# Kernel tuning notes

Hardware: AMD Instinct MI355X
Metric: run time of the kernel (lower is better)

Reference implementation:

```python
import jax, jax.numpy as jnp
import numpy as np
from jax import lax

HEADS = 4
DIM_HEAD = 32
IH = IW = 64
IH_RED = 32  # image_size // reduce_ratio; F.interpolate(size=int) -> square output


def dw_conv(t, w):
    # depthwise 3x3, stride 1, padding 1, NCHW; w: [C,1,3,3]
    return lax.conv_general_dilated(t, w, (1, 1), [(1, 1), (1, 1)],
                                    feature_group_count=t.shape[1],
                                    dimension_numbers=("NCHW", "OIHW", "NCHW"))


def pw_conv(t, w):
    # pointwise 1x1 conv as einsum; w: [O,C,1,1]
    return jnp.einsum("oc,bchw->bohw", w[:, :, 0, 0], t)


def resize_bilinear_ac(t, out_h, out_w):
    # bilinear, align_corners=True, t: [B,C,H,W]
    H, W = t.shape[-2], t.shape[-1]
    ys = jnp.linspace(0.0, H - 1.0, out_h)
    xs = jnp.linspace(0.0, W - 1.0, out_w)
    y0 = jnp.floor(ys).astype(jnp.int32)
    x0 = jnp.floor(xs).astype(jnp.int32)
    y1 = jnp.minimum(y0 + 1, H - 1)
    x1 = jnp.minimum(x0 + 1, W - 1)
    wy = (ys - y0).astype(t.dtype)[None, None, :, None]
    wx = (xs - x0).astype(t.dtype)[None, None, None, :]
    row = t[:, :, y0, :] * (1 - wy) + t[:, :, y1, :] * wy  # [B,C,OH,W]
    out = row[:, :, :, x0] * (1 - wx) + row[:, :, :, x1] * wx  # [B,C,OH,OW]
    return out


def to_heads(t):
    # [B, h*d, H, W] -> [B, h, H*W, d]
    B, _, H, W = t.shape
    return t.reshape(B, HEADS, DIM_HEAD, H * W).transpose(0, 1, 3, 2)


def setup_inputs() -> dict:
    key = jax.random.key(0)
    ks = jax.random.split(key, 7)
    inner = HEADS * DIM_HEAD  # 128
    return {
        "x": jax.random.normal(ks[0], (8, 256, 16, 16), jnp.float32),
        "skip": jax.random.normal(ks[1], (8, 128, 64, 64), jnp.float32),
        "dw_q": jax.random.normal(ks[2], (128, 1, 3, 3), jnp.float32) * 0.1,
        "pw_q": jax.random.normal(ks[3], (inner, 128, 1, 1), jnp.float32) * 0.05,
        "dw_kv": jax.random.normal(ks[4], (256, 1, 3, 3), jnp.float32) * 0.1,
        "pw_kv": jax.random.normal(ks[5], (2 * inner, 256, 1, 1), jnp.float32) * 0.05,
        "w_out": jax.random.normal(ks[6], (128, inner, 1, 1), jnp.float32) * 0.05,
    }


def reference(x, skip, dw_q, pw_q, dw_kv, pw_kv, w_out):
    scale = DIM_HEAD ** -0.5
    q = to_heads(pw_conv(dw_conv(skip, dw_q), pw_q))  # [B,h,4096,d]
    kv = pw_conv(dw_conv(x, dw_kv), pw_kv)            # [B,2*inner,16,16]
    k, v = jnp.split(kv, 2, axis=1)
    k = to_heads(resize_bilinear_ac(k, IH_RED, IH_RED))  # [B,h,1024,d]
    v = to_heads(resize_bilinear_ac(v, IH_RED, IH_RED))
    dots = jnp.einsum("bhqd,bhkd->bhqk", q, k) * scale
    attn = jax.nn.softmax(dots, axis=-1)
    out = jnp.einsum("bhqk,bhkd->bhqd", attn, v)  # [B,h,4096,d]
    B = out.shape[0]
    out = out.transpose(0, 1, 3, 2).reshape(B, HEADS * DIM_HEAD, IH, IW)
    return pw_conv(out, w_out)
```

## Files before the change

### kernel.cpp

```cpp
#include <hip/hip_runtime.h>
#include <hip/hip_bf16.h>

typedef __attribute__((ext_vector_type(4))) float f32x4;
typedef __attribute__((ext_vector_type(8))) short bf16x8;
typedef __attribute__((ext_vector_type(4))) unsigned u32x4;

#define DEV static __device__ __forceinline__

DEV int imin(int a, int b) { return a < b ? a : b; }

DEV short f2bf(float f) {
  union { float f; unsigned u; } v; v.f = f;
  unsigned r = (v.u + 0x7fffu + ((v.u >> 16) & 1u)) >> 16;
  return (short)r;
}

DEV unsigned pkbf(float lo, float hi) {
  unsigned r;
  asm("v_cvt_pk_bf16_f32 %0, %1, %2" : "=v"(r) : "v"(lo), "v"(hi));
  return r;
}

DEV bf16x8 cvt8(const float* __restrict__ p) {
  f32x4 a = *reinterpret_cast<const f32x4*>(p);
  f32x4 b = *reinterpret_cast<const f32x4*>(p + 4);
  bf16x8 r;
  r[0] = f2bf(a[0]); r[1] = f2bf(a[1]); r[2] = f2bf(a[2]); r[3] = f2bf(a[3]);
  r[4] = f2bf(b[0]); r[5] = f2bf(b[1]); r[6] = f2bf(b[2]); r[7] = f2bf(b[3]);
  return r;
}

DEV int sigma(int s) { return ((s & 4) << 2) | ((s >> 3) << 2) | (s & 3); }

__global__ __launch_bounds__(256) void k_dwq(const float* __restrict__ skip,
    const float* __restrict__ dw_q, short* __restrict__ dwQ) {
  const int b = blockIdx.z, cq = blockIdx.y, y = blockIdx.x;
  __shared__ __align__(16) short T[64][40];
  const int t = threadIdx.x;
  {
    const int x = t & 63, cg = t >> 6;
    #pragma unroll
    for (int i = 0; i < 8; ++i) {
      const int cl = cg * 8 + i;
      const int c = cq * 32 + cl;
      const float* sp = skip + (b * 128 + c) * 4096;
      const float* wp = dw_q + c * 9;
      float acc = 0.f;
      #pragma unroll
      for (int ky = 0; ky < 3; ++ky) {
        const int yy = y + ky - 1;
        if (yy < 0 || yy > 63) continue;
        #pragma unroll
        for (int kx = 0; kx < 3; ++kx) {
          const int xx = x + kx - 1;
          if (xx < 0 || xx > 63) continue;
          acc += sp[yy * 64 + xx] * wp[ky * 3 + kx];
        }
      }
      T[x][cl] = f2bf(acc);
    }
  }
  __syncthreads();
  const int x2 = t >> 2, cc = t & 3;
  bf16x8 v = *reinterpret_cast<const bf16x8*>(&T[x2][cc * 8]);
  *reinterpret_cast<bf16x8*>(dwQ + (b * 4096 + y * 64 + x2) * 128 + cq * 32 + cc * 8) = v;
}

__global__ __launch_bounds__(512) void k_kvgen(const float* __restrict__ x,
    const float* __restrict__ dw_kv, const float* __restrict__ pw_kv,
    float* __restrict__ kv16) {
  const int b = blockIdx.y;
  const int pq = blockIdx.x;
  __shared__ __align__(16) short dwxT[16][264];
  const int t = threadIdx.x;
  {
    const int pl = t & 15;
    const int cg = t >> 4;
    const int py = pq, px = pl;
    #pragma unroll
    for (int i = 0; i < 8; ++i) {
      const int c = cg * 8 + i;
      const float* sp = x + (b * 256 + c) * 256;
      const float* wp = dw_kv + c * 9;
      float acc = 0.f;
      #pragma unroll
      for (int ky = 0; ky < 3; ++ky) {
        const int yy = py + ky - 1;
        if (yy < 0 || yy > 15) continue;
        #pragma unroll
        for (int kx = 0; kx < 3; ++kx) {
          const int xx = px + kx - 1;
          if (xx < 0 || xx > 15) continue;
          acc += sp[yy * 16 + xx] * wp[ky * 3 + kx];
        }
      }
      dwxT[pl][c] = f2bf(acc);
    }
  }
  __syncthreads();
  const int w = t >> 6, l = t & 63, lr = l & 15, lg = l >> 4;
  f32x4 acc[2];
  #pragma unroll
  for (int ot = 0; ot < 2; ++ot) acc[ot] = f32x4{0.f, 0.f, 0.f, 0.f};
  #pragma unroll
  for (int kk = 0; kk < 8; ++kk) {
    const int c0 = kk * 32 + lg * 8;
    bf16x8 bfr = *reinterpret_cast<const bf16x8*>(&dwxT[lr][c0]);
    #pragma unroll
    for (int ot = 0; ot < 2; ++ot) {
      const int o = (w * 2 + ot) * 16 + lr;
      bf16x8 afr = cvt8(pw_kv + o * 256 + c0);
      acc[ot] = __builtin_amdgcn_mfma_f32_16x16x32_bf16(afr, bfr, acc[ot], 0, 0, 0);
    }
  }
  #pragma unroll
  for (int ot = 0; ot < 2; ++ot)
    #pragma unroll
    for (int r = 0; r < 4; ++r) {
      const int o = (w * 2 + ot) * 16 + lg * 4 + r;
      const int pix = pq * 16 + lr;
      kv16[(b * 256 + o) * 256 + pix] = acc[ot][r];
    }
}

DEV float bilin16(const float* __restrict__ p, int key) {
  const int oy = key >> 5, ox = key & 31;
  const float s = 15.f / 31.f;
  const float syf = oy * s, sxf = ox * s;
  const int y0 = (int)syf, x0 = (int)sxf;
  const int y1 = imin(y0 + 1, 15), x1 = imin(x0 + 1, 15);
  const float wy = syf - (float)y0, wx = sxf - (float)x0;
  const float r0 = p[y0 * 16 + x0] * (1.f - wx) + p[y0 * 16 + x1] * wx;
  const float r1 = p[y1 * 16 + x0] * (1.f - wx) + p[y1 * 16 + x1] * wx;
  return r0 * (1.f - wy) + r1 * wy;
}

__global__ __launch_bounds__(256) void k_resize(const float* __restrict__ kv16,
    short* __restrict__ Kp, short* __restrict__ Vp) {
  const int idx = blockIdx.x * 256 + threadIdx.x;
  {
    const int pos = idx & 31;
    int rest = idx >> 5;
    const int key = rest & 1023; rest >>= 10;
    const int h = rest & 3; const int b = rest >> 2;
    const int ch = h * 32 + sigma(pos);
    Kp[idx] = f2bf(bilin16(kv16 + (b * 256 + ch) * 256, key));
  }
  {
    const int keypos = idx & 1023;
    int rest = idx >> 10;
    const int d = rest & 31; rest >>= 5;
    const int h = rest & 3; const int b = rest >> 2;
    const int key = (keypos & ~31) | sigma(keypos & 31);
    const int ch = 128 + h * 32 + d;
    Vp[idx] = f2bf(bilin16(kv16 + (b * 256 + ch) * 256, key));
  }
}

__global__ __launch_bounds__(256) void k_attn(const short* __restrict__ dwQ,
    const float* __restrict__ pw_q, const short* __restrict__ Kp,
    const short* __restrict__ Vp, const float* __restrict__ w_out,
    float* __restrict__ out) {
  const int b = blockIdx.y;
  const int q0 = blockIdx.x * 32;
  const int t = threadIdx.x, h = t >> 6, l = t & 63;
  const int lr = l & 15, lg = l >> 4;
  __shared__ __align__(16) short QT[32][136];
  __shared__ __align__(16) short AT[32][136];

  {
    const int rr = t >> 4, c16 = t & 15;
    #pragma unroll
    for (int i = 0; i < 2; ++i) {
      const int q = rr + i * 16;
      bf16x8 v = *reinterpret_cast<const bf16x8*>(dwQ + (b * 4096 + q0 + q) * 128 + c16 * 8);
      *reinterpret_cast<bf16x8*>(&QT[q][c16 * 8]) = v;
    }
  }
  __syncthreads();

  bf16x8 qf[2];
  {
    f32x4 aq[2][2];
    #pragma unroll
    for (int ot = 0; ot < 2; ++ot)
      #pragma unroll
      for (int qt = 0; qt < 2; ++qt) aq[ot][qt] = f32x4{0.f, 0.f, 0.f, 0.f};
    #pragma unroll
    for (int kk = 0; kk < 4; ++kk) {
      const int c0 = kk * 32 + lg * 8;
      bf16x8 bfr[2];
      #pragma unroll
      for (int qt = 0; qt < 2; ++qt)
        bfr[qt] = *reinterpret_cast<const bf16x8*>(&QT[qt * 16 + lr][c0]);
      #pragma unroll
      for (int ot = 0; ot < 2; ++ot) {
        bf16x8 afr = cvt8(pw_q + ((h * 2 + ot) * 16 + lr) * 128 + c0);
        #pragma unroll
        for (int qt = 0; qt < 2; ++qt)
          aq[ot][qt] = __builtin_amdgcn_mfma_f32_16x16x32_bf16(afr, bfr[qt], aq[ot][qt], 0, 0, 0);
      }
    }
    const float qs = 0.25505403f;
    #pragma unroll
    for (int qt = 0; qt < 2; ++qt) {
      u32x4 qw;
      qw[0] = pkbf(aq[0][qt][0] * qs, aq[0][qt][1] * qs);
      qw[1] = pkbf(aq[0][qt][2] * qs, aq[0][qt][3] * qs);
      qw[2] = pkbf(aq[1][qt][0] * qs, aq[1][qt][1] * qs);
      qw[3] = pkbf(aq[1][qt][2] * qs, aq[1][qt][3] * qs);
      qf[qt] = *reinterpret_cast<bf16x8*>(&qw);
    }
  }

  const short* Kb = Kp + (b * 4 + h) * 32768;
  const short* Vb = Vp + (b * 4 + h) * 32768;
  f32x4 oacc[2][2];
  float ls[2];
  #pragma unroll
  for (int qt = 0; qt < 2; ++qt) {
    oacc[qt][0] = f32x4{0.f, 0.f, 0.f, 0.f};
    oacc[qt][1] = f32x4{0.f, 0.f, 0.f, 0.f};
    ls[qt] = 0.f;
  }
  for (int kc = 0; kc < 1024; kc += 32) {
    bf16x8 kf[2], vf[2];
    #pragma unroll
    for (int tt = 0; tt < 2; ++tt) {
      kf[tt] = *reinterpret_cast<const bf16x8*>(Kb + (kc + tt * 16 + lr) * 32 + lg * 8);
      vf[tt] = *reinterpret_cast<const bf16x8*>(Vb + (tt * 16 + lr) * 1024 + kc + lg * 8);
    }
    #pragma unroll
    for (int qt = 0; qt < 2; ++qt) {
      const f32x4 z = f32x4{0.f, 0.f, 0.f, 0.f};
      f32x4 s0 = __builtin_amdgcn_mfma_f32_16x16x32_bf16(kf[0], qf[qt], z, 0, 0, 0);
      f32x4 s1 = __builtin_amdgcn_mfma_f32_16x16x32_bf16(kf[1], qf[qt], z, 0, 0, 0);
      float p0[4], p1[4];
      #pragma unroll
      for (int r = 0; r < 4; ++r) {
        p0[r] = __builtin_amdgcn_exp2f(s0[r]);
        p1[r] = __builtin_amdgcn_exp2f(s1[r]);
      }
      ls[qt] += ((p0[0] + p0[1]) + (p0[2] + p0[3])) + ((p1[0] + p1[1]) + (p1[2] + p1[3]));
      u32x4 pw;
      pw[0] = pkbf(p0[0], p0[1]);
      pw[1] = pkbf(p0[2], p0[3]);
      pw[2] = pkbf(p1[0], p1[1]);
      pw[3] = pkbf(p1[2], p1[3]);
      bf16x8 pf = *reinterpret_cast<bf16x8*>(&pw);
      oacc[qt][0] = __builtin_amdgcn_mfma_f32_16x16x32_bf16(pf, vf[0], oacc[qt][0], 0, 0, 0);
      oacc[qt][1] = __builtin_amdgcn_mfma_f32_16x16x32_bf16(pf, vf[1], oacc[qt][1], 0, 0, 0);
    }
  }

  #pragma unroll
  for (int qt = 0; qt < 2; ++qt) {
    float s = ls[qt];
    s += __shfl_xor(s, 16);
    s += __shfl_xor(s, 32);
    const float inv = 1.f / s;
    #pragma unroll
    for (int r = 0; r < 4; ++r) {
      const float invr = __shfl(inv, lg * 4 + r);
      const int q = qt * 16 + lg * 4 + r;
      #pragma unroll
      for (int tt = 0; tt < 2; ++tt)
        AT[q][h * 32 + tt * 16 + lr] = f2bf(oacc[qt][tt][r] * invr);
    }
  }
  __syncthreads();

  f32x4 ao[2][2];
  #pragma unroll
  for (int jt = 0; jt < 2; ++jt)
    #pragma unroll
    for (int qt = 0; qt < 2; ++qt) ao[jt][qt] = f32x4{0.f, 0.f, 0.f, 0.f};
  #pragma unroll
  for (int kk = 0; kk < 4; ++kk) {
    const int c0 = kk * 32 + lg * 8;
    bf16x8 bfr[2];
    #pragma unroll
    for (int qt = 0; qt < 2; ++qt)
      bfr[qt] = *reinterpret_cast<const bf16x8*>(&AT[qt * 16 + lr][c0]);
    #pragma unroll
    for (int jt = 0; jt < 2; ++jt) {
      bf16x8 afr = cvt8(w_out + ((h * 2 + jt) * 16 + lr) * 128 + c0);
      #pragma unroll
      for (int qt = 0; qt < 2; ++qt)
        ao[jt][qt] = __builtin_amdgcn_mfma_f32_16x16x32_bf16(afr, bfr[qt], ao[jt][qt], 0, 0, 0);
    }
  }
  #pragma unroll
  for (int jt = 0; jt < 2; ++jt)
    #pragma unroll
    for (int qt = 0; qt < 2; ++qt)
      #pragma unroll
      for (int r = 0; r < 4; ++r) {
        const int j = (h * 2 + jt) * 16 + lg * 4 + r;
        out[(b * 128 + j) * 4096 + q0 + qt * 16 + lr] = ao[jt][qt][r];
      }
}

extern "C" void kernel_launch(void* const* d_in, const int* in_sizes, int n_in,
                              void* d_out, int out_size, void* d_ws, size_t ws_size,
                              hipStream_t stream) {
  const float* x     = (const float*)d_in[0];
  const float* skip  = (const float*)d_in[1];
  const float* dw_q  = (const float*)d_in[2];
  const float* pw_q  = (const float*)d_in[3];
  const float* dw_kv = (const float*)d_in[4];
  const float* pw_kv = (const float*)d_in[5];
  const float* w_out = (const float*)d_in[6];
  float* out = (float*)d_out;
  (void)in_sizes; (void)n_in; (void)out_size; (void)ws_size;

  char* wsb = (char*)d_ws;
  short* dwQ  = (short*)(wsb);
  float* kv16 = (float*)(wsb + (size_t)(8u << 20));
  short* Kp   = (short*)(wsb + (size_t)(10u << 20));
  short* Vp   = (short*)(wsb + (size_t)(12u << 20));

  k_dwq<<<dim3(64, 4, 8), dim3(256), 0, stream>>>(skip, dw_q, dwQ);
  k_kvgen<<<dim3(16, 8), dim3(512), 0, stream>>>(x, dw_kv, pw_kv, kv16);
  k_resize<<<dim3(4096), dim3(256), 0, stream>>>(kv16, Kp, Vp);
  k_attn<<<dim3(128, 8), dim3(256), 0, stream>>>(dwQ, pw_q, Kp, Vp, w_out, out);
}
```

Measured before the change: 194.2 us.

## Split attention keys across two wave groups and halve kvgen output per block

The attention kernel now launches 512 threads per block. Each head gets two waves, and each wave handles half of the 1024 keys. The partial outputs and row sums are combined through a shared-memory pool that is reused for Q, the partials and the output tile. The output projection is also spread over all eight waves. Separately, kvgen splits its output channels across an extra grid dimension, which raises block count but makes each block recompute the depthwise conv. The intent is more waves in flight and shorter per-wave serial loops, at the cost of extra barriers and shared-memory traffic for the reduction.

```diff
diff --git a/kernel.cpp b/kernel.cpp
--- a/kernel.cpp
+++ b/kernel.cpp
@@ -69,7 +69,8 @@
 __global__ __launch_bounds__(512) void k_kvgen(const float* __restrict__ x,
     const float* __restrict__ dw_kv, const float* __restrict__ pw_kv,
     float* __restrict__ kv16) {
-  const int b = blockIdx.y;
+  const int b = blockIdx.z;
+  const int oh = blockIdx.y;
   const int pq = blockIdx.x;
   __shared__ __align__(16) short dwxT[16][264];
   const int t = threadIdx.x;
@@ -99,28 +100,20 @@
   }
   __syncthreads();
   const int w = t >> 6, l = t & 63, lr = l & 15, lg = l >> 4;
-  f32x4 acc[2];
-  #pragma unroll
-  for (int ot = 0; ot < 2; ++ot) acc[ot] = f32x4{0.f, 0.f, 0.f, 0.f};
+  f32x4 acc = f32x4{0.f, 0.f, 0.f, 0.f};
+  const int o = oh * 128 + w * 16 + lr;
   #pragma unroll
   for (int kk = 0; kk < 8; ++kk) {
     const int c0 = kk * 32 + lg * 8;
     bf16x8 bfr = *reinterpret_cast<const bf16x8*>(&dwxT[lr][c0]);
-    #pragma unroll
-    for (int ot = 0; ot < 2; ++ot) {
-      const int o = (w * 2 + ot) * 16 + lr;
-      bf16x8 afr = cvt8(pw_kv + o * 256 + c0);
-      acc[ot] = __builtin_amdgcn_mfma_f32_16x16x32_bf16(afr, bfr, acc[ot], 0, 0, 0);
-    }
-  }
-  #pragma unroll
-  for (int ot = 0; ot < 2; ++ot)
-    #pragma unroll
-    for (int r = 0; r < 4; ++r) {
-      const int o = (w * 2 + ot) * 16 + lg * 4 + r;
-      const int pix = pq * 16 + lr;
-      kv16[(b * 256 + o) * 256 + pix] = acc[ot][r];
-    }
+    bf16x8 afr = cvt8(pw_kv + o * 256 + c0);
+    acc = __builtin_amdgcn_mfma_f32_16x16x32_bf16(afr, bfr, acc, 0, 0, 0);
+  }
+  #pragma unroll
+  for (int r = 0; r < 4; ++r) {
+    const int oo = oh * 128 + w * 16 + lg * 4 + r;
+    kv16[(b * 256 + oo) * 256 + pq * 16 + lr] = acc[r];
+  }
 }
 
 DEV float bilin16(const float* __restrict__ p, int key) {
@@ -157,25 +150,25 @@
   }
 }
 
-__global__ __launch_bounds__(256) void k_attn(const short* __restrict__ dwQ,
+__global__ __launch_bounds__(512, 8) void k_attn(const short* __restrict__ dwQ,
     const float* __restrict__ pw_q, const short* __restrict__ Kp,
     const short* __restrict__ Vp, const float* __restrict__ w_out,
     float* __restrict__ out) {
   const int b = blockIdx.y;
   const int q0 = blockIdx.x * 32;
-  const int t = threadIdx.x, h = t >> 6, l = t & 63;
+  const int t = threadIdx.x, w8 = t >> 6, l = t & 63;
+  const int h = w8 & 3, ks = w8 >> 2;
   const int lr = l & 15, lg = l >> 4;
-  __shared__ __align__(16) short QT[32][136];
-  __shared__ __align__(16) short AT[32][136];
-
-  {
-    const int rr = t >> 4, c16 = t & 15;
-    #pragma unroll
-    for (int i = 0; i < 2; ++i) {
-      const int q = rr + i * 16;
-      bf16x8 v = *reinterpret_cast<const bf16x8*>(dwQ + (b * 4096 + q0 + q) * 128 + c16 * 8);
-      *reinterpret_cast<bf16x8*>(&QT[q][c16 * 8]) = v;
-    }
+  __shared__ __align__(16) char POOL[33792];
+  short* QT = (short*)POOL;
+  float* Op = (float*)POOL;
+  float* Ls = (float*)(POOL + 32768);
+  short* AT = (short*)POOL;
+
+  {
+    const int q = t >> 4, c16 = t & 15;
+    bf16x8 v = *reinterpret_cast<const bf16x8*>(dwQ + (b * 4096 + q0 + q) * 128 + c16 * 8);
+    *reinterpret_cast<bf16x8*>(&QT[q * 136 + c16 * 8]) = v;
   }
   __syncthreads();
 
@@ -192,7 +185,7 @@
       bf16x8 bfr[2];
       #pragma unroll
       for (int qt = 0; qt < 2; ++qt)
-        bfr[qt] = *reinterpret_cast<const bf16x8*>(&QT[qt * 16 + lr][c0]);
+        bfr[qt] = *reinterpret_cast<const bf16x8*>(&QT[(qt * 16 + lr) * 136 + c0]);
       #pragma unroll
       for (int ot = 0; ot < 2; ++ot) {
         bf16x8 afr = cvt8(pw_q + ((h * 2 + ot) * 16 + lr) * 128 + c0);
@@ -212,6 +205,7 @@
       qf[qt] = *reinterpret_cast<bf16x8*>(&qw);
     }
   }
+  __syncthreads();
 
   const short* Kb = Kp + (b * 4 + h) * 32768;
   const short* Vb = Vp + (b * 4 + h) * 32768;
@@ -223,7 +217,8 @@
     oacc[qt][1] = f32x4{0.f, 0.f, 0.f, 0.f};
     ls[qt] = 0.f;
   }
-  for (int kc = 0; kc < 1024; kc += 32) {
+  const int kend = ks * 512 + 512;
+  for (int kc = ks * 512; kc < kend; kc += 32) {
     bf16x8 kf[2], vf[2];
     #pragma unroll
     for (int tt = 0; tt < 2; ++tt) {
@@ -258,47 +253,55 @@
     float s = ls[qt];
     s += __shfl_xor(s, 16);
     s += __shfl_xor(s, 32);
-    const float inv = 1.f / s;
-    #pragma unroll
-    for (int r = 0; r < 4; ++r) {
-      const float invr = __shfl(inv, lg * 4 + r);
-      const int q = qt * 16 + lg * 4 + r;
-      #pragma unroll
-      for (int tt = 0; tt < 2; ++tt)
-        AT[q][h * 32 + tt * 16 + lr] = f2bf(oacc[qt][tt][r] * invr);
-    }
-  }
-  __syncthreads();
-
-  f32x4 ao[2][2];
-  #pragma unroll
-  for (int jt = 0; jt < 2; ++jt)
-    #pragma unroll
-    for (int qt = 0; qt < 2; ++qt) ao[jt][qt] = f32x4{0.f, 0.f, 0.f, 0.f};
+    if (lg == 0) Ls[w8 * 32 + qt * 16 + lr] = s;
+    #pragma unroll
+    for (int tt = 0; tt < 2; ++tt)
+      #pragma unroll
+      for (int r = 0; r < 4; ++r)
+        Op[w8 * 1024 + (qt * 16 + lg * 4 + r) * 32 + tt * 16 + lr] = oacc[qt][tt][r];
+  }
+  __syncthreads();
+
+  const int mq = l >> 1, md = ks * 16 + (l & 1) * 8;
+  bf16x8 atv;
+  {
+    const f32x4* OpV = (const f32x4*)POOL;
+    f32x4 a0 = OpV[(h * 1024 + mq * 32 + md) >> 2];
+    f32x4 a1 = OpV[(h * 1024 + mq * 32 + md + 4) >> 2];
+    f32x4 b0 = OpV[((4 + h) * 1024 + mq * 32 + md) >> 2];
+    f32x4 b1 = OpV[((4 + h) * 1024 + mq * 32 + md + 4) >> 2];
+    const float inv = 1.f / (Ls[h * 32 + mq] + Ls[(4 + h) * 32 + mq]);
+    f32x4 va = (a0 + b0) * inv;
+    f32x4 vb = (a1 + b1) * inv;
+    u32x4 pk;
+    pk[0] = pkbf(va[0], va[1]); pk[1] = pkbf(va[2], va[3]);
+    pk[2] = pkbf(vb[0], vb[1]); pk[3] = pkbf(vb[2], vb[3]);
+    atv = *reinterpret_cast<bf16x8*>(&pk);
+  }
+  __syncthreads();
+  *reinterpret_cast<bf16x8*>(&AT[mq * 136 + h * 32 + md]) = atv;
+  __syncthreads();
+
+  f32x4 ao[2];
+  ao[0] = f32x4{0.f, 0.f, 0.f, 0.f};
+  ao[1] = f32x4{0.f, 0.f, 0.f, 0.f};
   #pragma unroll
   for (int kk = 0; kk < 4; ++kk) {
     const int c0 = kk * 32 + lg * 8;
-    bf16x8 bfr[2];
-    #pragma unroll
-    for (int qt = 0; qt < 2; ++qt)
-      bfr[qt] = *reinterpret_cast<const bf16x8*>(&AT[qt * 16 + lr][c0]);
-    #pragma unroll
-    for (int jt = 0; jt < 2; ++jt) {
-      bf16x8 afr = cvt8(w_out + ((h * 2 + jt) * 16 + lr) * 128 + c0);
-      #pragma unroll
-      for (int qt = 0; qt < 2; ++qt)
-        ao[jt][qt] = __builtin_amdgcn_mfma_f32_16x16x32_bf16(afr, bfr[qt], ao[jt][qt], 0, 0, 0);
-    }
-  }
-  #pragma unroll
-  for (int jt = 0; jt < 2; ++jt)
-    #pragma unroll
-    for (int qt = 0; qt < 2; ++qt)
-      #pragma unroll
-      for (int r = 0; r < 4; ++r) {
-        const int j = (h * 2 + jt) * 16 + lg * 4 + r;
-        out[(b * 128 + j) * 4096 + q0 + qt * 16 + lr] = ao[jt][qt][r];
-      }
+    bf16x8 afr = cvt8(w_out + (w8 * 16 + lr) * 128 + c0);
+    #pragma unroll
+    for (int qt = 0; qt < 2; ++qt) {
+      bf16x8 bfr = *reinterpret_cast<const bf16x8*>(&AT[(qt * 16 + lr) * 136 + c0]);
+      ao[qt] = __builtin_amdgcn_mfma_f32_16x16x32_bf16(afr, bfr, ao[qt], 0, 0, 0);
+    }
+  }
+  #pragma unroll
+  for (int qt = 0; qt < 2; ++qt)
+    #pragma unroll
+    for (int r = 0; r < 4; ++r) {
+      const int j = w8 * 16 + lg * 4 + r;
+      out[(b * 128 + j) * 4096 + q0 + qt * 16 + lr] = ao[qt][r];
+    }
 }
 
 extern "C" void kernel_launch(void* const* d_in, const int* in_sizes, int n_in,
@@ -321,7 +324,7 @@
   short* Vp   = (short*)(wsb + (size_t)(12u << 20));
 
   k_dwq<<<dim3(64, 4, 8), dim3(256), 0, stream>>>(skip, dw_q, dwQ);
-  k_kvgen<<<dim3(16, 8), dim3(512), 0, stream>>>(x, dw_kv, pw_kv, kv16);
+  k_kvgen<<<dim3(16, 2, 8), dim3(512), 0, stream>>>(x, dw_kv, pw_kv, kv16);
   k_resize<<<dim3(4096), dim3(256), 0, stream>>>(kv16, Kp, Vp);
-  k_attn<<<dim3(128, 8), dim3(256), 0, stream>>>(dwQ, pw_q, Kp, Vp, w_out, out);
-}
+  k_attn<<<dim3(128, 8), dim3(512), 0, stream>>>(dwQ, pw_q, Kp, Vp, w_out, out);
+}
```

Measured after the change: 272.1 us. +40.1%, slower.
